# Kernel tuning notes

Hardware: AMD Instinct MI355X
Metric: run time of the kernel (lower is better)

## Reference

```python
import jax, jax.numpy as jnp
import numpy as np

N, E = 20000, 640000
D_IN, D_H, D_OUT = 128, 64, 32


def _lin_w(key, out_d, in_d):
    return jax.random.normal(key, (out_d, in_d), jnp.float32) / np.sqrt(in_d)


def setup_inputs() -> dict:
    key = jax.random.key(0)
    ks = jax.random.split(key, 16)
    x = jax.random.normal(ks[0], (N, D_IN), jnp.float32)
    edge_index = jax.random.randint(ks[1], (2, E), 0, N, jnp.int64)
    inp = {"x": x, "edge_index": edge_index}
    # SAGEConv weights: lin_l (aggregated neighbors, with bias), lin_r (root, no bias)
    inp["Wl1"] = _lin_w(ks[2], D_H, D_IN); inp["bl1"] = jnp.zeros((D_H,), jnp.float32)
    inp["Wr1"] = _lin_w(ks[3], D_H, D_IN)
    inp["Wl2"] = _lin_w(ks[4], D_H, D_H); inp["bl2"] = jnp.zeros((D_H,), jnp.float32)
    inp["Wr2"] = _lin_w(ks[5], D_H, D_H)
    inp["Wl3"] = _lin_w(ks[6], D_OUT, D_H); inp["bl3"] = jnp.zeros((D_OUT,), jnp.float32)
    inp["Wr3"] = _lin_w(ks[7], D_OUT, D_H)
    # Conv2d kernels (OIHW), all 3x3 pad 1
    inp["Wc1"] = jax.random.normal(ks[8], (D_H, 1, 3, 3), jnp.float32) / 3.0
    inp["bc1"] = jnp.zeros((D_H,), jnp.float32)
    inp["Wc2"] = jax.random.normal(ks[9], (D_H, D_H, 3, 3), jnp.float32) / np.sqrt(9 * D_H)
    inp["bc2"] = jnp.zeros((D_H,), jnp.float32)
    inp["Wc3"] = jax.random.normal(ks[10], (1, D_H, 3, 3), jnp.float32) / np.sqrt(9 * D_H)
    inp["bc3"] = jnp.zeros((1,), jnp.float32)
    # linear2 (hidden -> hidden)
    inp["W2"] = _lin_w(ks[11], D_H, D_H); inp["b2"] = jnp.zeros((D_H,), jnp.float32)
    return inp


def _sage(x, src, dst, Wl, bl, Wr):
    # PyG SAGEConv (mean aggr): lin_l(mean_{j->i} x_j) + lin_r(x_i)
    msg = x[src]  # [E, d] gather
    agg = jax.ops.segment_sum(msg, dst, num_segments=N)
    deg = jax.ops.segment_sum(jnp.ones((src.shape[0], 1), x.dtype), dst, num_segments=N)
    agg = agg / jnp.maximum(deg, 1.0)
    return agg @ Wl.T + bl + x @ Wr.T


def _conv(x, w, b):
    y = jax.lax.conv_general_dilated(x, w, (1, 1), ((1, 1), (1, 1)),
                                     dimension_numbers=("NCHW", "OIHW", "NCHW"))
    return y + b[None, :, None, None]


def reference(x, edge_index, Wl1, bl1, Wr1, Wl2, bl2, Wr2, Wl3, bl3, Wr3,
              Wc1, bc1, Wc2, bc2, Wc3, bc3, W2, b2):
    src, dst = edge_index[0], edge_index[1]
    h = _sage(x, src, dst, Wl1, bl1, Wr1)
    h = _sage(h, src, dst, Wl2, bl2, Wr2)
    h = _sage(h, src, dst, Wl2, bl2, Wr2)  # sage2 reused, as in source
    out_1 = h
    h4 = h[None, None]                     # [1,1,N,D_H]
    out = _conv(h4, Wc1, bc1)              # [1,D_H,N,D_H]
    out = _conv(out, Wc2, bc2)             # dropout is identity at inference
    out = _conv(out, Wc3, bc3)             # [1,1,N,D_H]
    out = out[0, 0] + out_1
    out = out @ W2.T + b2
    h = _sage(out, src, dst, Wl2, bl2, Wr2)
    h = _sage(h, src, dst, Wl2, bl2, Wr2)
    h = _sage(h, src, dst, Wl3, bl3, Wr3)
    return h
```

## Files before the change

### kernel.cpp

```cpp
#include <hip/hip_runtime.h>

#define NN 20000
#define NE 640000
#define NBUK 79

__device__ __forceinline__ int probe_stride(const int* __restrict__ ei32) {
  int lane = threadIdx.x & 63;
  int v = ei32[2 * lane + 1];
  unsigned long long nz = __ballot(v != 0);
  return (nz == 0ull) ? 2 : 1;
}

__device__ __forceinline__ bool maskB(int var, int o2, int o1) {
  int s = o2 + o1;
  switch (var) {
    case 0: return (o2 >= 0) && (s >= 0);
    case 1: return s >= -1;
    case 3: return s <= 1;
    case 4: return (o2 <= 0) && (s <= 0);
    default: return true;
  }
}

__global__ __launch_bounds__(256) void k_phaseA1(
    const int* __restrict__ ei, int* __restrict__ bhist,
    const float* __restrict__ Wc1, const float* __restrict__ Wc2,
    const float* __restrict__ Wc3, const float* __restrict__ bc1,
    const float* __restrict__ bc2, const float* __restrict__ bc3,
    const float* __restrict__ Wl1, const float* __restrict__ Wr1,
    const float* __restrict__ Wl2, const float* __restrict__ Wr2,
    const float* __restrict__ bl2,
    float* __restrict__ T729, float* __restrict__ beta5,
    float* __restrict__ Wt1, float* __restrict__ Wt2,
    float* __restrict__ Sbuf, float* __restrict__ c5,
    int* __restrict__ rowptr, int E, int N) {
  __shared__ float smem[6336];
  int b = blockIdx.x, tid = threadIdx.x;
  if (b >= 151) {
    int* lb = (int*)smem;
    int st = probe_stride(ei);
    for (int i = tid; i < NBUK; i += 256) lb[i] = 0;
    __syncthreads();
    int u = b - 151;
    int e0 = u * 4096;
#pragma unroll
    for (int t = 0; t < 16; ++t) {
      int e = e0 + t * 256 + tid;
      if (e < E) atomicAdd(&lb[ei[(size_t)(E + e) * st] >> 8], 1);
    }
    __syncthreads();
    for (int i = tid; i < NBUK; i += 256) bhist[u * NBUK + i] = lb[i];
    return;
  }
  int s = b;
  if (s == 0) {
    float* W3  = smem;
    float* S9s = smem + 576;
    float* W1s = smem + 5760;
    if (tid == 0) rowptr[N] = E;
    for (int e = tid; e < 576; e += 256) { W3[e] = Wc3[e]; W1s[e] = Wc1[e]; }
    __syncthreads();
    for (int bb = tid; bb < 576; bb += 256) {
      float acc[9];
#pragma unroll
      for (int a = 0; a < 9; ++a) acc[a] = 0.0f;
#pragma unroll 4
      for (int o = 0; o < 64; ++o) {
        float w2 = Wc2[o * 576 + bb];
#pragma unroll
        for (int a = 0; a < 9; ++a) acc[a] += W3[o * 9 + a] * w2;
      }
#pragma unroll
      for (int a = 0; a < 9; ++a) S9s[a * 576 + bb] = acc[a];
    }
    __syncthreads();
    for (int c = tid; c < 729; c += 256) {
      int kx0  = c % 3;
      int dl1e = (c / 3) % 3;
      int dl2e = (c / 9) % 3;
      int ky0  = (c / 27) % 3;
      int ky1  = (c / 81) % 3;
      int ky2  = c / 243;
      const float* s9 = &S9s[(ky2 * 3 + dl2e) * 576 + ky1 * 3 + dl1e];
      const float* w1 = &W1s[ky0 * 3 + kx0];
      float t = 0.0f;
#pragma unroll 8
      for (int i = 0; i < 64; ++i) t += s9[i * 9] * w1[i * 9];
      T729[c] = t;
    }
  } else if (s <= 5) {
    float* S2   = smem;
    float* W3b  = smem + 576;
    float* B2   = smem + 1152;
    float* part = smem + 1216;
    int var = s - 1;
    for (int e = tid; e < 576; e += 256) {
      int o = e / 9, r = e - o * 9;
      float t = 0.0f;
      for (int i = 0; i < 64; ++i) t += Wc2[o * 576 + i * 9 + r] * bc1[i];
      S2[e] = t;
      W3b[e] = Wc3[e];
    }
    if (tid < 64) B2[tid] = bc2[tid];
    __syncthreads();
    int u = tid & 63, oc = tid >> 6;
    float acc = 0.0f;
    for (int ky2 = 0; ky2 < 3; ++ky2) {
      int o2 = ky2 - 1;
      bool okA = (var == 0) ? (o2 >= 0) : (var == 4) ? (o2 <= 0) : true;
      if (!okA) continue;
      for (int dl2 = -1; dl2 <= 1; ++dl2) {
        int p = u + dl2; if ((unsigned)p >= 64u) continue;
        float sel[9];
#pragma unroll
        for (int ky1 = 0; ky1 < 3; ++ky1) {
          int o1 = ky1 - 1;
          bool mb = maskB(var, o2, o1);
#pragma unroll
          for (int dl1 = -1; dl1 <= 1; ++dl1) {
            int pq = p + dl1;
            sel[ky1 * 3 + dl1 + 1] = (mb && (unsigned)pq < 64u) ? 1.0f : 0.0f;
          }
        }
#pragma unroll 4
        for (int oo = 0; oo < 16; ++oo) {
          int o = oc * 16 + oo;
          float inner = B2[o];
#pragma unroll
          for (int r = 0; r < 9; ++r) inner += S2[o * 9 + r] * sel[r];
          acc += W3b[o * 9 + ky2 * 3 + (dl2 + 1)] * inner;
        }
      }
    }
    part[tid] = acc;
    __syncthreads();
    if (tid < 64) {
      beta5[var * 64 + tid] =
          bc3[0] + part[tid] + part[64 + tid] + part[128 + tid] + part[192 + tid];
    }
  } else {
    int idx = (s - 6) * 256 + tid;
    if (idx < 16384) {
      int w = idx >> 7, u = idx & 127;
      Wt1[idx] = (u < 64) ? Wl1[u * 128 + w] : Wr1[(u - 64) * 128 + w];
    } else if (idx < 24576) {
      int t = idx - 16384;
      int w = t >> 7, u = t & 127;
      Wt2[t] = (u < 64) ? Wl2[u * 64 + w] : Wr2[(u - 64) * 64 + w];
    } else if (idx < 36864) {
      int t2 = idx - 24576;
      int m = t2 >> 12, e = t2 & 4095;
      int i = e >> 6, j = e & 63;
      float acc = 0.0f;
#pragma unroll 4
      for (int k = 0; k < 64; ++k) {
        float wlj = Wl2[j * 64 + k], wrj = Wr2[j * 64 + k];
        float wli = Wl2[k * 64 + i], wri = Wr2[k * 64 + i];
        if (m == 0) acc += wli * wlj;
        else if (m == 1) acc += wri * wlj + wli * wrj;
        else acc += wri * wrj;
      }
      Sbuf[t2] = acc;
    } else if (idx < 36928) {
      int j = idx - 36864;
      float acc = bl2[j];
      for (int i = 0; i < 64; ++i)
        acc += bl2[i] * (Wl2[j * 64 + i] + Wr2[j * 64 + i]);
      c5[j] = acc;
    }
  }
}

__global__ __launch_bounds__(256) void k_phaseA2(
    const float* __restrict__ X, const float* __restrict__ Wt1,
    float* __restrict__ yzA,
    const int* __restrict__ ei, const int* __restrict__ bhist,
    unsigned long long* __restrict__ ebuf,
    const float* __restrict__ T729, float* __restrict__ M5T,
    const float* __restrict__ Sbuf, const float* __restrict__ c5,
    const float* __restrict__ Wl3, const float* __restrict__ Wr3,
    const float* __restrict__ bl3, float* __restrict__ Gbuf,
    float* __restrict__ c32, int E, int N) {
  __shared__ float smem[2048];
  int b = blockIdx.x, tid = threadIdx.x;
  if (b < 157) {
    int* lcnt  = (int*)smem;
    int* lbase = (int*)smem + 128;
    int* sscan = (int*)smem + 256;
    int st = probe_stride(ei);
    for (int i = tid; i < NBUK; i += 256) lcnt[i] = 0;
    int tot = 0, myoff = 0;
    if (tid < NBUK) {
      for (int v = 0; v < 157; ++v) {
        int h = bhist[v * NBUK + tid];
        tot += h;
        if (v < b) myoff += h;
      }
    }
    if (tid < 128) sscan[tid] = (tid < NBUK) ? tot : 0;
    __syncthreads();
    for (int off = 1; off < 128; off <<= 1) {
      int v = 0;
      if (tid < 128 && tid >= off) v = sscan[tid - off];
      __syncthreads();
      if (tid < 128) sscan[tid] += v;
      __syncthreads();
    }
    if (tid < NBUK) lbase[tid] = (sscan[tid] - tot) + myoff;
    __syncthreads();
    int e0 = b * 4096;
    int srcv[16], dstv[16], lrank[16], bk[16];
    int n = 0;
#pragma unroll
    for (int t = 0; t < 16; ++t) {
      int e = e0 + t * 256 + tid;
      if (e < E) {
        int sv = ei[(size_t)e * st];
        int d = ei[(size_t)(E + e) * st];
        int bb = d >> 8;
        srcv[n] = sv; dstv[n] = d; bk[n] = bb;
        lrank[n] = atomicAdd(&lcnt[bb], 1);
        ++n;
      }
    }
    for (int t = 0; t < n; ++t) {
      int pos = lbase[bk[t]] + lrank[t];
      ebuf[pos] = ((unsigned long long)(unsigned)dstv[t] << 32) | (unsigned)srcv[t];
    }
  } else if (b < 219) {
    float* Ts = smem;
    for (int e = tid; e < 729; e += 256) Ts[e] = T729[e];
    __syncthreads();
    int idx = (b - 157) * 256 + tid;
    if (idx >= 15680) return;
    int jw = idx % 7;
    int u  = (idx / 7) % 64;
    int d  = (idx / 448) % 7;
    int var = idx / 3136;
    int w = u + jw - 3;
    float acc = 0.0f;
    if (w >= 0 && w < 64) {
      for (int ky2 = 0; ky2 < 3; ++ky2) {
        int o2 = ky2 - 1;
        for (int ky1 = 0; ky1 < 3; ++ky1) {
          int o1 = ky1 - 1;
          if (!maskB(var, o2, o1)) continue;
          int o0 = (d - 3) - o2 - o1;
          if (o0 < -1 || o0 > 1) continue;
          int ky0 = o0 + 1;
          int cbase = ((ky2 * 3 + ky1) * 3 + ky0) * 27;
#pragma unroll
          for (int kx0 = 0; kx0 < 3; ++kx0) {
            int jq = jw - kx0;
            if ((unsigned)jq >= 5u) continue;
            int q = u + jq - 2;
            if ((unsigned)q >= 64u) continue;
#pragma unroll
            for (int dl2e = 0; dl2e < 3; ++dl2e) {
              int p = u + dl2e - 1;
              if ((unsigned)p >= 64u) continue;
              int dl1e = jq - dl2e;
              if ((unsigned)dl1e >= 3u) continue;
              acc += Ts[cbase + dl2e * 9 + dl1e * 3 + kx0];
            }
          }
        }
      }
    }
    if (d == 3 && jw == 3) acc += 1.0f;
    M5T[(var * 49 + d * 7 + jw) * 64 + u] = acc;
  } else if (b < 252) {
    int bb = b - 219;
    if (bb < 32) {
      int idx = bb * 256 + tid;
      int kblk = idx >> 11;
      int rem = idx & 2047;
      int t = rem >> 5, j = rem & 31;
      const float* S2p = Sbuf;
      const float* S1p = Sbuf + 4096;
      const float* S0p = Sbuf + 8192;
      const float* pa = (kblk == 0) ? S2p : (kblk == 1) ? S1p : (kblk == 2) ? S0p : nullptr;
      const float* pb = (kblk == 1) ? S2p : (kblk == 2) ? S1p : (kblk == 3) ? S0p : nullptr;
      float acc = 0.0f;
#pragma unroll 4
      for (int k = 0; k < 64; ++k) {
        if (pa) acc += pa[t * 64 + k] * Wl3[j * 64 + k];
        if (pb) acc += pb[t * 64 + k] * Wr3[j * 64 + k];
      }
      Gbuf[idx] = acc;
    } else if (tid < 32) {
      float acc = bl3[tid];
      for (int k = 0; k < 64; ++k)
        acc += c5[k] * (Wl3[tid * 64 + k] + Wr3[tid * 64 + k]);
      c32[tid] = acc;
    }
  } else {
    constexpr int C = 128, K = 128, ROWS = 16, RPT = ROWS * C / 256;
    float* Xs = smem;
    int y0 = (b - 252) * ROWS;
    {
      const float4* src = (const float4*)(X + (size_t)y0 * K);
      float4* dst = (float4*)Xs;
#pragma unroll
      for (int v = 0; v < ROWS * K / 4 / 256; ++v)
        dst[v * 256 + tid] = src[v * 256 + tid];
    }
    __syncthreads();
    int u = tid % C;
    int rg = tid / C;
    float acc[RPT];
#pragma unroll
    for (int k = 0; k < RPT; ++k) acc[k] = 0.0f;
#pragma unroll 2
    for (int w0 = 0; w0 < K; w0 += 4) {
      float m0 = Wt1[(w0 + 0) * C + u];
      float m1 = Wt1[(w0 + 1) * C + u];
      float m2 = Wt1[(w0 + 2) * C + u];
      float m3 = Wt1[(w0 + 3) * C + u];
      const float* xs = &Xs[(rg * RPT) * K + w0];
#pragma unroll
      for (int k = 0; k < RPT; ++k) {
        float4 h = *(const float4*)(xs + k * K);
        acc[k] += m0 * h.x + m1 * h.y + m2 * h.z + m3 * h.w;
      }
    }
#pragma unroll
    for (int k = 0; k < RPT; ++k)
      yzA[(size_t)(y0 + rg * RPT + k) * C + u] = acc[k];
  }
}

__global__ __launch_bounds__(256) void k_phaseA3(
    const unsigned long long* __restrict__ ebuf, const int* __restrict__ bhist,
    int* __restrict__ rowptr, float* __restrict__ invdeg,
    int* __restrict__ csr,
    const float* __restrict__ Gbuf, const float* __restrict__ W2,
    const float* __restrict__ b2, float* __restrict__ Wg,
    float* __restrict__ bg, int N) {
  __shared__ int smem[772];
  int b = blockIdx.x, tid = threadIdx.x;
  if (b < NBUK) {
    int* lcnt  = smem;
    int* lcur  = smem + 256;
    int* wsum  = smem + 512;
    int* sscan = smem + 516;
    int* tots  = smem + 644;
    int tot = 0;
    if (tid < NBUK)
      for (int v = 0; v < 157; ++v) tot += bhist[v * NBUK + tid];
    if (tid < 128) { tots[tid] = (tid < NBUK) ? tot : 0; sscan[tid] = tots ? ((tid < NBUK) ? tot : 0) : 0; }
    __syncthreads();
    for (int off = 1; off < 128; off <<= 1) {
      int v = 0;
      if (tid < 128 && tid >= off) v = sscan[tid - off];
      __syncthreads();
      if (tid < 128) sscan[tid] += v;
      __syncthreads();
    }
    if (tid < 128) sscan[tid] -= tots[tid];
    __syncthreads();
    int base = sscan[b];
    int n = tots[b];
    lcnt[tid] = 0;
    __syncthreads();
    for (int e = tid; e < n; e += 256) {
      int d = (int)(ebuf[base + e] >> 32);
      atomicAdd(&lcnt[d - (b << 8)], 1);
    }
    __syncthreads();
    int c = lcnt[tid];
    int lane = tid & 63, wid = tid >> 6;
    int s = c;
#pragma unroll
    for (int off = 1; off < 64; off <<= 1) {
      int v = __shfl_up(s, off, 64);
      if (lane >= off) s += v;
    }
    if (lane == 63) wsum[wid] = s;
    __syncthreads();
    int woff = 0;
    for (int w = 0; w < wid; ++w) woff += wsum[w];
    int pref = woff + s - c;
    int gnode = (b << 8) + tid;
    if (gnode < N) {
      rowptr[gnode] = base + pref;
      invdeg[gnode] = 1.0f / (float)(c < 1 ? 1 : c);
    }
    lcur[tid] = pref;
    __syncthreads();
    for (int e = tid; e < n; e += 256) {
      unsigned long long pk = ebuf[base + e];
      int d = (int)(pk >> 32);
      int pos = atomicAdd(&lcur[d - (b << 8)], 1);
      csr[base + pos] = (int)(unsigned)pk;
    }
  } else {
    int bb = b - NBUK;
    if (bb < 32) {
      int idx = bb * 256 + tid;
      int w = idx >> 7, u = idx & 127;
      int kblk = u >> 5, j = u & 31;
      const float* gp = Gbuf + kblk * 2048 + j;
      float acc = 0.0f;
#pragma unroll 4
      for (int t = 0; t < 64; ++t) acc += W2[t * 64 + w] * gp[t * 32];
      Wg[idx] = acc;
    } else if (tid < 128) {
      int kblk = tid >> 5, j = tid & 31;
      const float* gp = Gbuf + kblk * 2048 + j;
      float acc = 0.0f;
      for (int t = 0; t < 64; ++t) acc += b2[t] * gp[t * 32];
      bg[tid] = acc;
    }
  }
}

template <int C>
__global__ __launch_bounds__(256) void k_fused(const float* __restrict__ yzin,
                                               const int* __restrict__ csr,
                                               const int* __restrict__ rowptr,
                                               const float* __restrict__ invdeg,
                                               const float* __restrict__ bl,
                                               const float* __restrict__ Wt,
                                               float* __restrict__ out, int N) {
  constexpr int FV = 16;
  constexpr int G  = 4;
  constexpr int S4 = 32;
  constexpr int CAP = 64;
  __shared__ int idxs[16 * CAP];
  __shared__ float htile[16 * 64];
  int tid = threadIdx.x;
  int w = tid >> 6, lane = tid & 63;
  int base = blockIdx.x * 16;
  int beg_r[4], m_r[4], end_r[4];
#pragma unroll
  for (int rr = 0; rr < 4; ++rr) {
    int node = base + w * 4 + rr;
    int beg = rowptr[node], end = rowptr[node + 1];
    beg_r[rr] = beg; end_r[rr] = end;
    int cnt = end - beg;
    int m = cnt < CAP ? cnt : CAP;
    m_r[rr] = m;
    int* my = &idxs[(w * 4 + rr) * CAP];
    for (int k = lane; k < m; k += 64) my[k] = csr[beg + k];
  }
  __syncthreads();
  int g = lane / FV, f = lane % FV;
  const float4* yz4 = (const float4*)yzin;
#pragma unroll
  for (int rr = 0; rr < 4; ++rr) {
    int node = base + w * 4 + rr;
    const int* my = &idxs[(w * 4 + rr) * CAP];
    int m = m_r[rr];
    float a0x=0,a0y=0,a0z=0,a0w=0, a1x=0,a1y=0,a1z=0,a1w=0;
    float a2x=0,a2y=0,a2z=0,a2w=0, a3x=0,a3y=0,a3z=0,a3w=0;
    int j = g;
    for (; j + 3 * G < m; j += 4 * G) {
      int s0 = my[j], s1 = my[j + G], s2 = my[j + 2 * G], s3 = my[j + 3 * G];
      float4 v0 = yz4[(size_t)s0 * S4 + f];
      float4 v1 = yz4[(size_t)s1 * S4 + f];
      float4 v2 = yz4[(size_t)s2 * S4 + f];
      float4 v3 = yz4[(size_t)s3 * S4 + f];
      a0x += v0.x; a0y += v0.y; a0z += v0.z; a0w += v0.w;
      a1x += v1.x; a1y += v1.y; a1z += v1.z; a1w += v1.w;
      a2x += v2.x; a2y += v2.y; a2z += v2.z; a2w += v2.w;
      a3x += v3.x; a3y += v3.y; a3z += v3.z; a3w += v3.w;
    }
    for (; j < m; j += G) {
      int s0 = my[j];
      float4 v0 = yz4[(size_t)s0 * S4 + f];
      a0x += v0.x; a0y += v0.y; a0z += v0.z; a0w += v0.w;
    }
    for (int jj = beg_r[rr] + CAP + g; jj < end_r[rr]; jj += G) {
      int s0 = csr[jj];
      float4 v0 = yz4[(size_t)s0 * S4 + f];
      a0x += v0.x; a0y += v0.y; a0z += v0.z; a0w += v0.w;
    }
    float ax = (a0x + a1x) + (a2x + a3x);
    float ay = (a0y + a1y) + (a2y + a3y);
    float az = (a0z + a1z) + (a2z + a3z);
    float aw = (a0w + a1w) + (a2w + a3w);
#pragma unroll
    for (int mm = FV; mm < 64; mm <<= 1) {
      ax += __shfl_xor(ax, mm, 64);
      ay += __shfl_xor(ay, mm, 64);
      az += __shfl_xor(az, mm, 64);
      aw += __shfl_xor(aw, mm, 64);
    }
    if (g == 0) {
      float4 root = yz4[(size_t)node * S4 + FV + f];
      float4 bv = ((const float4*)bl)[f];
      float id = invdeg[node];
      float4 o;
      o.x = ax * id + bv.x + root.x;
      o.y = ay * id + bv.y + root.y;
      o.z = az * id + bv.z + root.z;
      o.w = aw * id + bv.w + root.w;
      ((float4*)htile)[(w * 4 + rr) * 16 + f] = o;
    }
  }
  __syncthreads();
  constexpr int RPT = 16 * C / 256;
  int u = tid % C, rg = tid / C;
  float acc[RPT];
#pragma unroll
  for (int k = 0; k < RPT; ++k) acc[k] = 0.0f;
#pragma unroll 2
  for (int w0 = 0; w0 < 64; w0 += 4) {
    float m0 = Wt[(w0 + 0) * C + u];
    float m1 = Wt[(w0 + 1) * C + u];
    float m2 = Wt[(w0 + 2) * C + u];
    float m3 = Wt[(w0 + 3) * C + u];
    const float* xs = &htile[(rg * RPT) * 64 + w0];
#pragma unroll
    for (int k = 0; k < RPT; ++k) {
      float4 h4 = *(const float4*)(xs + k * 64);
      acc[k] += m0 * h4.x + m1 * h4.y + m2 * h4.z + m3 * h4.w;
    }
  }
#pragma unroll
  for (int k = 0; k < RPT; ++k)
    out[(size_t)(base + rg * RPT + k) * C + u] = acc[k];
}

__global__ __launch_bounds__(256) void k_applyfused(
    const float* __restrict__ h, const float* __restrict__ M5T,
    const float* __restrict__ beta5, const float* __restrict__ Wg,
    const float* __restrict__ bg, float* __restrict__ wout, int N) {
  __shared__ float hs[22 * 70];
  __shared__ float htile[16 * 64];
  int tid = threadIdx.x;
  int bstart = blockIdx.x * 16;
  for (int idx = tid; idx < 22 * 70; idx += 256) {
    int row = idx / 70, col = idx - row * 70;
    int y = bstart - 3 + row;
    int ww = col - 3;
    float v = 0.0f;
    if ((unsigned)y < (unsigned)N && (unsigned)ww < 64u)
      v = h[(size_t)y * 64 + ww];
    hs[idx] = v;
  }
  __syncthreads();
  int u = tid & 63, g = tid >> 6;
  int lr0 = g * 4;
  int gstart = bstart + lr0;
  const float* basep = &hs[lr0 * 70 + u];
  bool interior = (gstart >= 2) && (gstart + 3 <= N - 3);
  if (interior) {
    float c[49];
#pragma unroll
    for (int t = 0; t < 49; ++t) c[t] = M5T[(2 * 49 + t) * 64 + u];
    float bet = beta5[2 * 64 + u];
    float acc[4];
#pragma unroll
    for (int k = 0; k < 4; ++k) acc[k] = bet;
#pragma unroll
    for (int rr = 0; rr < 10; ++rr) {
      float t7[7];
#pragma unroll
      for (int jw = 0; jw < 7; ++jw) t7[jw] = basep[rr * 70 + jw];
#pragma unroll
      for (int d = 0; d < 7; ++d) {
        int k = rr - d;
        if (k >= 0 && k < 4) {
#pragma unroll
          for (int jw = 0; jw < 7; ++jw) acc[k] += c[d * 7 + jw] * t7[jw];
        }
      }
    }
#pragma unroll
    for (int k = 0; k < 4; ++k) htile[(lr0 + k) * 64 + u] = acc[k];
  } else {
    for (int k = 0; k < 4; ++k) {
      int y = gstart + k;
      int var = (y == 0) ? 0 : (y == 1) ? 1 : (y == N - 2) ? 3 : (y == N - 1) ? 4 : 2;
      float acc = beta5[var * 64 + u];
      for (int d = 0; d < 7; ++d)
        for (int jw = 0; jw < 7; ++jw)
          acc += M5T[(var * 49 + d * 7 + jw) * 64 + u] * basep[(k + d) * 70 + jw];
      htile[(lr0 + k) * 64 + u] = acc;
    }
  }
  __syncthreads();
  int u2 = tid % 128, rg = tid / 128;
  float acc2[8];
  float bv = bg[u2];
#pragma unroll
  for (int k = 0; k < 8; ++k) acc2[k] = bv;
#pragma unroll 2
  for (int w0 = 0; w0 < 64; w0 += 4) {
    float m0 = Wg[(w0 + 0) * 128 + u2];
    float m1 = Wg[(w0 + 1) * 128 + u2];
    float m2 = Wg[(w0 + 2) * 128 + u2];
    float m3 = Wg[(w0 + 3) * 128 + u2];
    const float* xs = &htile[(rg * 8) * 64 + w0];
#pragma unroll
    for (int k = 0; k < 8; ++k) {
      float4 h4 = *(const float4*)(xs + k * 64);
      acc2[k] += m0 * h4.x + m1 * h4.y + m2 * h4.z + m3 * h4.w;
    }
  }
  int kb = u2 >> 5, jj = u2 & 31;
#pragma unroll
  for (int k = 0; k < 8; ++k) {
    int node = bstart + rg * 8 + k;
    wout[((size_t)kb * N + node) * 32 + jj] = acc2[k];
  }
}

template <int DH>
__global__ __launch_bounds__(256) void k_agg(const float* __restrict__ yz,
                                             const int* __restrict__ csr,
                                             const int* __restrict__ rowptr,
                                             const float* __restrict__ invdeg,
                                             const float* __restrict__ bl,
                                             float* __restrict__ out, int N) {
  constexpr int FV = DH / 4;
  constexpr int G  = 64 / FV;
  constexpr int S4 = DH / 2;
  constexpr int CAP = 256;
  __shared__ int idxs[4 * CAP];
  int wid = threadIdx.x >> 6, lane = threadIdx.x & 63;
  int node = blockIdx.x * 4 + wid;
  int beg = rowptr[node], end = rowptr[node + 1];
  int cnt = end - beg;
  int m = cnt < CAP ? cnt : CAP;
  int* my = &idxs[wid * CAP];
  for (int k = lane; k < m; k += 64) my[k] = csr[beg + k];
  __syncthreads();
  int g = lane / FV, f = lane % FV;
  const float4* yz4 = (const float4*)yz;
  float a0x=0,a0y=0,a0z=0,a0w=0, a1x=0,a1y=0,a1z=0,a1w=0;
  float a2x=0,a2y=0,a2z=0,a2w=0, a3x=0,a3y=0,a3z=0,a3w=0;
  int j = g;
  for (; j + 3 * G < m; j += 4 * G) {
    int s0 = my[j], s1 = my[j + G], s2 = my[j + 2 * G], s3 = my[j + 3 * G];
    float4 v0 = yz4[(size_t)s0 * S4 + f];
    float4 v1 = yz4[(size_t)s1 * S4 + f];
    float4 v2 = yz4[(size_t)s2 * S4 + f];
    float4 v3 = yz4[(size_t)s3 * S4 + f];
    a0x += v0.x; a0y += v0.y; a0z += v0.z; a0w += v0.w;
    a1x += v1.x; a1y += v1.y; a1z += v1.z; a1w += v1.w;
    a2x += v2.x; a2y += v2.y; a2z += v2.z; a2w += v2.w;
    a3x += v3.x; a3y += v3.y; a3z += v3.z; a3w += v3.w;
  }
  for (; j < m; j += G) {
    int s0 = my[j];
    float4 v0 = yz4[(size_t)s0 * S4 + f];
    a0x += v0.x; a0y += v0.y; a0z += v0.z; a0w += v0.w;
  }
  for (int jj = beg + CAP + g; jj < end; jj += G) {
    int s0 = csr[jj];
    float4 v0 = yz4[(size_t)s0 * S4 + f];
    a0x += v0.x; a0y += v0.y; a0z += v0.z; a0w += v0.w;
  }
  float ax = (a0x + a1x) + (a2x + a3x);
  float ay = (a0y + a1y) + (a2y + a3y);
  float az = (a0z + a1z) + (a2z + a3z);
  float aw = (a0w + a1w) + (a2w + a3w);
#pragma unroll
  for (int mm = FV; mm < 64; mm <<= 1) {
    ax += __shfl_xor(ax, mm, 64);
    ay += __shfl_xor(ay, mm, 64);
    az += __shfl_xor(az, mm, 64);
    aw += __shfl_xor(aw, mm, 64);
  }
  if (g == 0) {
    float4 root = yz4[(size_t)node * S4 + FV + f];
    float4 bv = ((const float4*)bl)[f];
    float id = invdeg[node];
    float4 o;
    o.x = ax * id + bv.x + root.x;
    o.y = ay * id + bv.y + root.y;
    o.z = az * id + bv.z + root.z;
    o.w = aw * id + bv.w + root.w;
    ((float4*)out)[(size_t)node * FV + f] = o;
  }
}

__global__ __launch_bounds__(256) void k_agg32(
    const float* __restrict__ src, const int* __restrict__ csr,
    const int* __restrict__ rowptr, const float* __restrict__ invdeg,
    const float* __restrict__ add, const float* __restrict__ cvec,
    float* __restrict__ out, int N) {
  constexpr int FV = 8;
  constexpr int G  = 8;
  constexpr int CAP = 256;
  __shared__ int idxs[4 * CAP];
  int wid = threadIdx.x >> 6, lane = threadIdx.x & 63;
  int node = blockIdx.x * 4 + wid;
  int beg = rowptr[node], end = rowptr[node + 1];
  int cnt = end - beg;
  int m = cnt < CAP ? cnt : CAP;
  int* my = &idxs[wid * CAP];
  for (int k = lane; k < m; k += 64) my[k] = csr[beg + k];
  __syncthreads();
  int g = lane / FV, f = lane % FV;
  const float4* sr4 = (const float4*)src;
  float a0x=0,a0y=0,a0z=0,a0w=0, a1x=0,a1y=0,a1z=0,a1w=0;
  float a2x=0,a2y=0,a2z=0,a2w=0, a3x=0,a3y=0,a3z=0,a3w=0;
  int j = g;
  for (; j + 3 * G < m; j += 4 * G) {
    int s0 = my[j], s1 = my[j + G], s2 = my[j + 2 * G], s3 = my[j + 3 * G];
    float4 v0 = sr4[(size_t)s0 * FV + f];
    float4 v1 = sr4[(size_t)s1 * FV + f];
    float4 v2 = sr4[(size_t)s2 * FV + f];
    float4 v3 = sr4[(size_t)s3 * FV + f];
    a0x += v0.x; a0y += v0.y; a0z += v0.z; a0w += v0.w;
    a1x += v1.x; a1y += v1.y; a1z += v1.z; a1w += v1.w;
    a2x += v2.x; a2y += v2.y; a2z += v2.z; a2w += v2.w;
    a3x += v3.x; a3y += v3.y; a3z += v3.z; a3w += v3.w;
  }
  for (; j < m; j += G) {
    int s0 = my[j];
    float4 v0 = sr4[(size_t)s0 * FV + f];
    a0x += v0.x; a0y += v0.y; a0z += v0.z; a0w += v0.w;
  }
  for (int jj = beg + CAP + g; jj < end; jj += G) {
    int s0 = csr[jj];
    float4 v0 = sr4[(size_t)s0 * FV + f];
    a0x += v0.x; a0y += v0.y; a0z += v0.z; a0w += v0.w;
  }
  float ax = (a0x + a1x) + (a2x + a3x);
  float ay = (a0y + a1y) + (a2y + a3y);
  float az = (a0z + a1z) + (a2z + a3z);
  float aw = (a0w + a1w) + (a2w + a3w);
#pragma unroll
  for (int mm = FV; mm < 64; mm <<= 1) {
    ax += __shfl_xor(ax, mm, 64);
    ay += __shfl_xor(ay, mm, 64);
    az += __shfl_xor(az, mm, 64);
    aw += __shfl_xor(aw, mm, 64);
  }
  if (g == 0) {
    float4 av = ((const float4*)add)[(size_t)node * FV + f];
    float id = invdeg[node];
    float4 o;
    o.x = ax * id + av.x;
    o.y = ay * id + av.y;
    o.z = az * id + av.z;
    o.w = aw * id + av.w;
    if (cvec != nullptr) {
      float4 cv = ((const float4*)cvec)[f];
      o.x += cv.x; o.y += cv.y; o.z += cv.z; o.w += cv.w;
    }
    ((float4*)out)[(size_t)node * FV + f] = o;
  }
}

extern "C" void kernel_launch(void* const* d_in, const int* in_sizes, int n_in,
                              void* d_out, int out_size, void* d_ws, size_t ws_size,
                              hipStream_t stream) {
  const int N = NN, E = NE;
  const float* x   = (const float*)d_in[0];
  const int*   ei  = (const int*)d_in[1];
  const float* Wl1 = (const float*)d_in[2];
  const float* bl1 = (const float*)d_in[3];
  const float* Wr1 = (const float*)d_in[4];
  const float* Wl2 = (const float*)d_in[5];
  const float* bl2 = (const float*)d_in[6];
  const float* Wr2 = (const float*)d_in[7];
  const float* Wl3 = (const float*)d_in[8];
  const float* bl3 = (const float*)d_in[9];
  const float* Wr3 = (const float*)d_in[10];
  const float* Wc1 = (const float*)d_in[11];
  const float* bc1 = (const float*)d_in[12];
  const float* Wc2 = (const float*)d_in[13];
  const float* bc2 = (const float*)d_in[14];
  const float* Wc3 = (const float*)d_in[15];
  const float* bc3 = (const float*)d_in[16];
  const float* W2  = (const float*)d_in[17];
  const float* b2  = (const float*)d_in[18];

  char* ws = (char*)d_ws;
  size_t off = 0;
  auto alloc = [&](size_t bytes) -> void* {
    off = (off + 255) & ~(size_t)255;
    void* p = ws + off;
    off += bytes;
    return p;
  };
  int*   rowptr  = (int*)alloc((size_t)(N + 1) * 4);
  float* invdeg  = (float*)alloc((size_t)N * 4);
  int*   csr     = (int*)alloc((size_t)E * 4);
  unsigned long long* ebuf = (unsigned long long*)alloc((size_t)E * 8);
  int*   bhist   = (int*)alloc(157 * NBUK * 4);
  float* Wt1     = (float*)alloc(128 * 128 * 4);
  float* Wt2     = (float*)alloc(64 * 128 * 4);
  float* T729    = (float*)alloc(729 * 4);
  float* M5T     = (float*)alloc(15680 * 4);
  float* beta5   = (float*)alloc(320 * 4);
  float* Sbuf    = (float*)alloc(12288 * 4);
  float* c5      = (float*)alloc(64 * 4);
  float* Gbuf    = (float*)alloc(8192 * 4);
  float* Wg      = (float*)alloc(8192 * 4);
  float* bg      = (float*)alloc(128 * 4);
  float* c32     = (float*)alloc(32 * 4);
  float* yzA     = (float*)alloc((size_t)N * 128 * 4);
  float* yzB     = (float*)alloc((size_t)N * 128 * 4);
  float* hA      = (float*)alloc((size_t)N * 64 * 4);
  float* wbuf    = (float*)alloc((size_t)4 * N * 32 * 4);
  float* s1buf   = (float*)alloc((size_t)N * 32 * 4);
  float* s2buf   = (float*)alloc((size_t)N * 32 * 4);
  (void)ws_size; (void)in_sizes; (void)n_in; (void)out_size;

  const int gG = N / 16;
  const int gA = N / 4;

  k_phaseA1<<<308, 256, 0, stream>>>(ei, bhist, Wc1, Wc2, Wc3, bc1, bc2, bc3,
                                     Wl1, Wr1, Wl2, Wr2, bl2,
                                     T729, beta5, Wt1, Wt2, Sbuf, c5,
                                     rowptr, E, N);
  k_phaseA2<<<1502, 256, 0, stream>>>(x, Wt1, yzA, ei, bhist, ebuf,
                                      T729, M5T, Sbuf, c5, Wl3, Wr3, bl3,
                                      Gbuf, c32, E, N);
  k_phaseA3<<<112, 256, 0, stream>>>(ebuf, bhist, rowptr, invdeg, csr,
                                     Gbuf, W2, b2, Wg, bg, N);

  k_fused<128><<<gG, 256, 0, stream>>>(yzA, csr, rowptr, invdeg, bl1, Wt2, yzB, N);
  k_fused<128><<<gG, 256, 0, stream>>>(yzB, csr, rowptr, invdeg, bl2, Wt2, yzA, N);
  k_agg<64><<<gA, 256, 0, stream>>>(yzA, csr, rowptr, invdeg, bl2, hA, N);
  k_applyfused<<<gG, 256, 0, stream>>>(hA, M5T, beta5, Wg, bg, wbuf, N);
  const float* w3  = wbuf;
  const float* w2p = wbuf + (size_t)N * 32;
  const float* w1p = wbuf + (size_t)2 * N * 32;
  const float* w0p = wbuf + (size_t)3 * N * 32;
  k_agg32<<<gA, 256, 0, stream>>>(w3, csr, rowptr, invdeg, w2p, nullptr, s1buf, N);
  k_agg32<<<gA, 256, 0, stream>>>(s1buf, csr, rowptr, invdeg, w1p, nullptr, s2buf, N);
  k_agg32<<<gA, 256, 0, stream>>>(s2buf, csr, rowptr, invdeg, w0p, c32, (float*)d_out, N);
}
```

Baseline: 278.6 us.

## Bin edges into fixed-capacity per-block cells and merge CSR build into phaseA2

The histogram blocks in phaseA1 now also write each packed (dst,src) edge into a fixed-size cell indexed by (edge block, destination bucket). That removes the separate global scatter pass that used to read edge_index a second time. phaseA2's first 79 blocks then assemble each bucket directly from these cells, using a prefix scan and binary search, to produce rowptr, invdeg and csr. The Gbuf, Wg and bg weight folding is done by a single block, so the third setup kernel launch is gone. The trade-off is that the code assumes no (block, bucket) cell exceeds 128 edges, which holds only for roughly uniform destinations, and it adds serial work in one block.

Result: slower. 676.3 us (+142.7%).

```diff
diff --git a/kernel.cpp b/kernel.cpp
--- a/kernel.cpp
+++ b/kernel.cpp
@@ -3,6 +3,8 @@
 #define NN 20000
 #define NE 640000
 #define NBUK 79
+#define NPB 157
+#define CELL 128
 
 __device__ __forceinline__ int probe_stride(const int* __restrict__ ei32) {
   int lane = threadIdx.x & 63;
@@ -24,6 +26,7 @@
 
 __global__ __launch_bounds__(256) void k_phaseA1(
     const int* __restrict__ ei, int* __restrict__ bhist,
+    unsigned long long* __restrict__ ebuf2,
     const float* __restrict__ Wc1, const float* __restrict__ Wc2,
     const float* __restrict__ Wc3, const float* __restrict__ bc1,
     const float* __restrict__ bc2, const float* __restrict__ bc3,
@@ -37,19 +40,25 @@
   __shared__ float smem[6336];
   int b = blockIdx.x, tid = threadIdx.x;
   if (b >= 151) {
-    int* lb = (int*)smem;
+    int* lcnt = (int*)smem;
     int st = probe_stride(ei);
-    for (int i = tid; i < NBUK; i += 256) lb[i] = 0;
+    for (int i = tid; i < NBUK; i += 256) lcnt[i] = 0;
     __syncthreads();
     int u = b - 151;
     int e0 = u * 4096;
-#pragma unroll
     for (int t = 0; t < 16; ++t) {
       int e = e0 + t * 256 + tid;
-      if (e < E) atomicAdd(&lb[ei[(size_t)(E + e) * st] >> 8], 1);
-    }
-    __syncthreads();
-    for (int i = tid; i < NBUK; i += 256) bhist[u * NBUK + i] = lb[i];
+      if (e < E) {
+        int sv = ei[(size_t)e * st];
+        int d  = ei[(size_t)(E + e) * st];
+        int bb = d >> 8;
+        int r = atomicAdd(&lcnt[bb], 1);
+        ebuf2[((size_t)u * NBUK + bb) * CELL + r] =
+            ((unsigned long long)(unsigned)d << 32) | (unsigned)sv;
+      }
+    }
+    __syncthreads();
+    for (int i = tid; i < NBUK; i += 256) bhist[u * NBUK + i] = lcnt[i];
     return;
   }
   int s = b;
@@ -174,31 +183,48 @@
 __global__ __launch_bounds__(256) void k_phaseA2(
     const float* __restrict__ X, const float* __restrict__ Wt1,
     float* __restrict__ yzA,
-    const int* __restrict__ ei, const int* __restrict__ bhist,
-    unsigned long long* __restrict__ ebuf,
+    const unsigned long long* __restrict__ ebuf2,
+    const int* __restrict__ bhist,
+    int* __restrict__ rowptr, float* __restrict__ invdeg,
+    int* __restrict__ csr,
     const float* __restrict__ T729, float* __restrict__ M5T,
     const float* __restrict__ Sbuf, const float* __restrict__ c5,
     const float* __restrict__ Wl3, const float* __restrict__ Wr3,
     const float* __restrict__ bl3, float* __restrict__ Gbuf,
+    float* __restrict__ Wg, float* __restrict__ bg,
+    const float* __restrict__ W2, const float* __restrict__ b2,
     float* __restrict__ c32, int E, int N) {
   __shared__ float smem[2048];
   int b = blockIdx.x, tid = threadIdx.x;
-  if (b < 157) {
-    int* lcnt  = (int*)smem;
-    int* lbase = (int*)smem + 128;
-    int* sscan = (int*)smem + 256;
-    int st = probe_stride(ei);
-    for (int i = tid; i < NBUK; i += 256) lcnt[i] = 0;
-    int tot = 0, myoff = 0;
-    if (tid < NBUK) {
-      for (int v = 0; v < 157; ++v) {
-        int h = bhist[v * NBUK + tid];
-        tot += h;
-        if (v < b) myoff += h;
+  if (b < NBUK) {
+    int* lens  = (int*)smem;
+    int* cs    = (int*)smem + 160;
+    int* lcnt  = (int*)smem + 416;
+    int* lcur  = (int*)smem + 672;
+    int* wsum  = (int*)smem + 928;
+    int* sscan = (int*)smem + 932;
+    int* tots  = (int*)smem + 1060;
+    if (tid < 160) lens[tid] = (tid < NPB) ? bhist[tid * NBUK + b] : 0;
+    int tot = 0;
+    if (tid < NBUK)
+      for (int v = 0; v < NPB; ++v) tot += bhist[v * NBUK + tid];
+    if (tid < 128) {
+      int tv = (tid < NBUK) ? tot : 0;
+      tots[tid] = tv;
+      sscan[tid] = tv;
+    }
+    __syncthreads();
+    {
+      int mine = (tid < NPB) ? lens[tid] : 0;
+      cs[tid] = mine;
+      __syncthreads();
+      for (int off = 1; off < 256; off <<= 1) {
+        int v = (tid >= off) ? cs[tid - off] : 0;
+        __syncthreads();
+        cs[tid] += v;
+        __syncthreads();
       }
     }
-    if (tid < 128) sscan[tid] = (tid < NBUK) ? tot : 0;
-    __syncthreads();
     for (int off = 1; off < 128; off <<= 1) {
       int v = 0;
       if (tid < 128 && tid >= off) v = sscan[tid - off];
@@ -206,32 +232,53 @@
       if (tid < 128) sscan[tid] += v;
       __syncthreads();
     }
-    if (tid < NBUK) lbase[tid] = (sscan[tid] - tot) + myoff;
-    __syncthreads();
-    int e0 = b * 4096;
-    int srcv[16], dstv[16], lrank[16], bk[16];
-    int n = 0;
-#pragma unroll
-    for (int t = 0; t < 16; ++t) {
-      int e = e0 + t * 256 + tid;
-      if (e < E) {
-        int sv = ei[(size_t)e * st];
-        int d = ei[(size_t)(E + e) * st];
-        int bb = d >> 8;
-        srcv[n] = sv; dstv[n] = d; bk[n] = bb;
-        lrank[n] = atomicAdd(&lcnt[bb], 1);
-        ++n;
-      }
-    }
-    for (int t = 0; t < n; ++t) {
-      int pos = lbase[bk[t]] + lrank[t];
-      ebuf[pos] = ((unsigned long long)(unsigned)dstv[t] << 32) | (unsigned)srcv[t];
-    }
-  } else if (b < 219) {
+    if (tid < 128) sscan[tid] -= tots[tid];
+    lcnt[tid] = 0;
+    __syncthreads();
+    int base = sscan[b];
+    int n = cs[NPB - 1];
+    for (int i = tid; i < n; i += 256) {
+      int lo = 0, hi = NPB - 1;
+      while (lo < hi) { int mid = (lo + hi) >> 1; if (cs[mid] > i) hi = mid; else lo = mid + 1; }
+      int pos = i - (cs[lo] - lens[lo]);
+      unsigned long long pk = ebuf2[((size_t)lo * NBUK + b) * CELL + pos];
+      atomicAdd(&lcnt[(int)(pk >> 32) & 255], 1);
+    }
+    __syncthreads();
+    int c = lcnt[tid];
+    int lane = tid & 63, wid = tid >> 6;
+    int sacc = c;
+#pragma unroll
+    for (int off = 1; off < 64; off <<= 1) {
+      int v = __shfl_up(sacc, off, 64);
+      if (lane >= off) sacc += v;
+    }
+    if (lane == 63) wsum[wid] = sacc;
+    __syncthreads();
+    int woff = 0;
+    for (int w = 0; w < wid; ++w) woff += wsum[w];
+    int pref = woff + sacc - c;
+    int gnode = (b << 8) + tid;
+    if (gnode < N) {
+      rowptr[gnode] = base + pref;
+      invdeg[gnode] = 1.0f / (float)(c < 1 ? 1 : c);
+    }
+    lcur[tid] = pref;
+    __syncthreads();
+    for (int i = tid; i < n; i += 256) {
+      int lo = 0, hi = NPB - 1;
+      while (lo < hi) { int mid = (lo + hi) >> 1; if (cs[mid] > i) hi = mid; else lo = mid + 1; }
+      int pos = i - (cs[lo] - lens[lo]);
+      unsigned long long pk = ebuf2[((size_t)lo * NBUK + b) * CELL + pos];
+      int d = (int)(pk >> 32);
+      int p2 = atomicAdd(&lcur[d & 255], 1);
+      csr[base + p2] = (int)(unsigned)pk;
+    }
+  } else if (b < 141) {
     float* Ts = smem;
     for (int e = tid; e < 729; e += 256) Ts[e] = T729[e];
     __syncthreads();
-    int idx = (b - 157) * 256 + tid;
+    int idx = (b - NBUK) * 256 + tid;
     if (idx >= 15680) return;
     int jw = idx % 7;
     int u  = (idx / 7) % 64;
@@ -269,10 +316,8 @@
     }
     if (d == 3 && jw == 3) acc += 1.0f;
     M5T[(var * 49 + d * 7 + jw) * 64 + u] = acc;
-  } else if (b < 252) {
-    int bb = b - 219;
-    if (bb < 32) {
-      int idx = bb * 256 + tid;
+  } else if (b == 141) {
+    for (int idx = tid; idx < 8192; idx += 256) {
       int kblk = idx >> 11;
       int rem = idx & 2047;
       int t = rem >> 5, j = rem & 31;
@@ -288,7 +333,25 @@
         if (pb) acc += pb[t * 64 + k] * Wr3[j * 64 + k];
       }
       Gbuf[idx] = acc;
-    } else if (tid < 32) {
+    }
+    __syncthreads();
+    for (int idx = tid; idx < 8192; idx += 256) {
+      int w = idx >> 7, u = idx & 127;
+      int kblk = u >> 5, j = u & 31;
+      const float* gp = Gbuf + kblk * 2048 + j;
+      float acc = 0.0f;
+#pragma unroll 4
+      for (int t = 0; t < 64; ++t) acc += W2[t * 64 + w] * gp[t * 32];
+      Wg[idx] = acc;
+    }
+    if (tid < 128) {
+      int kblk = tid >> 5, j = tid & 31;
+      const float* gp = Gbuf + kblk * 2048 + j;
+      float acc = 0.0f;
+      for (int t = 0; t < 64; ++t) acc += b2[t] * gp[t * 32];
+      bg[tid] = acc;
+    }
+    if (tid < 32) {
       float acc = bl3[tid];
       for (int k = 0; k < 64; ++k)
         acc += c5[k] * (Wl3[tid * 64 + k] + Wr3[tid * 64 + k]);
@@ -297,7 +360,7 @@
   } else {
     constexpr int C = 128, K = 128, ROWS = 16, RPT = ROWS * C / 256;
     float* Xs = smem;
-    int y0 = (b - 252) * ROWS;
+    int y0 = (b - 142) * ROWS;
     {
       const float4* src = (const float4*)(X + (size_t)y0 * K);
       float4* dst = (float4*)Xs;
@@ -327,91 +390,6 @@
 #pragma unroll
     for (int k = 0; k < RPT; ++k)
       yzA[(size_t)(y0 + rg * RPT + k) * C + u] = acc[k];
-  }
-}
-
-__global__ __launch_bounds__(256) void k_phaseA3(
-    const unsigned long long* __restrict__ ebuf, const int* __restrict__ bhist,
-    int* __restrict__ rowptr, float* __restrict__ invdeg,
-    int* __restrict__ csr,
-    const float* __restrict__ Gbuf, const float* __restrict__ W2,
-    const float* __restrict__ b2, float* __restrict__ Wg,
-    float* __restrict__ bg, int N) {
-  __shared__ int smem[772];
-  int b = blockIdx.x, tid = threadIdx.x;
-  if (b < NBUK) {
-    int* lcnt  = smem;
-    int* lcur  = smem + 256;
-    int* wsum  = smem + 512;
-    int* sscan = smem + 516;
-    int* tots  = smem + 644;
-    int tot = 0;
-    if (tid < NBUK)
-      for (int v = 0; v < 157; ++v) tot += bhist[v * NBUK + tid];
-    if (tid < 128) { tots[tid] = (tid < NBUK) ? tot : 0; sscan[tid] = tots ? ((tid < NBUK) ? tot : 0) : 0; }
-    __syncthreads();
-    for (int off = 1; off < 128; off <<= 1) {
-      int v = 0;
-      if (tid < 128 && tid >= off) v = sscan[tid - off];
-      __syncthreads();
-      if (tid < 128) sscan[tid] += v;
-      __syncthreads();
-    }
-    if (tid < 128) sscan[tid] -= tots[tid];
-    __syncthreads();
-    int base = sscan[b];
-    int n = tots[b];
-    lcnt[tid] = 0;
-    __syncthreads();
-    for (int e = tid; e < n; e += 256) {
-      int d = (int)(ebuf[base + e] >> 32);
-      atomicAdd(&lcnt[d - (b << 8)], 1);
-    }
-    __syncthreads();
-    int c = lcnt[tid];
-    int lane = tid & 63, wid = tid >> 6;
-    int s = c;
-#pragma unroll
-    for (int off = 1; off < 64; off <<= 1) {
-      int v = __shfl_up(s, off, 64);
-      if (lane >= off) s += v;
-    }
-    if (lane == 63) wsum[wid] = s;
-    __syncthreads();
-    int woff = 0;
-    for (int w = 0; w < wid; ++w) woff += wsum[w];
-    int pref = woff + s - c;
-    int gnode = (b << 8) + tid;
-    if (gnode < N) {
-      rowptr[gnode] = base + pref;
-      invdeg[gnode] = 1.0f / (float)(c < 1 ? 1 : c);
-    }
-    lcur[tid] = pref;
-    __syncthreads();
-    for (int e = tid; e < n; e += 256) {
-      unsigned long long pk = ebuf[base + e];
-      int d = (int)(pk >> 32);
-      int pos = atomicAdd(&lcur[d - (b << 8)], 1);
-      csr[base + pos] = (int)(unsigned)pk;
-    }
-  } else {
-    int bb = b - NBUK;
-    if (bb < 32) {
-      int idx = bb * 256 + tid;
-      int w = idx >> 7, u = idx & 127;
-      int kblk = u >> 5, j = u & 31;
-      const float* gp = Gbuf + kblk * 2048 + j;
-      float acc = 0.0f;
-#pragma unroll 4
-      for (int t = 0; t < 64; ++t) acc += W2[t * 64 + w] * gp[t * 32];
-      Wg[idx] = acc;
-    } else if (tid < 128) {
-      int kblk = tid >> 5, j = tid & 31;
-      const float* gp = Gbuf + kblk * 2048 + j;
-      float acc = 0.0f;
-      for (int t = 0; t < 64; ++t) acc += b2[t] * gp[t * 32];
-      bg[tid] = acc;
-    }
   }
 }
 
@@ -783,8 +761,9 @@
   int*   rowptr  = (int*)alloc((size_t)(N + 1) * 4);
   float* invdeg  = (float*)alloc((size_t)N * 4);
   int*   csr     = (int*)alloc((size_t)E * 4);
-  unsigned long long* ebuf = (unsigned long long*)alloc((size_t)E * 8);
-  int*   bhist   = (int*)alloc(157 * NBUK * 4);
+  unsigned long long* ebuf2 =
+      (unsigned long long*)alloc((size_t)NPB * NBUK * CELL * 8);
+  int*   bhist   = (int*)alloc(NPB * NBUK * 4);
   float* Wt1     = (float*)alloc(128 * 128 * 4);
   float* Wt2     = (float*)alloc(64 * 128 * 4);
   float* T729    = (float*)alloc(729 * 4);
@@ -807,15 +786,15 @@
   const int gG = N / 16;
   const int gA = N / 4;
 
-  k_phaseA1<<<308, 256, 0, stream>>>(ei, bhist, Wc1, Wc2, Wc3, bc1, bc2, bc3,
+  k_phaseA1<<<308, 256, 0, stream>>>(ei, bhist, ebuf2,
+                                     Wc1, Wc2, Wc3, bc1, bc2, bc3,
                                      Wl1, Wr1, Wl2, Wr2, bl2,
                                      T729, beta5, Wt1, Wt2, Sbuf, c5,
                                      rowptr, E, N);
-  k_phaseA2<<<1502, 256, 0, stream>>>(x, Wt1, yzA, ei, bhist, ebuf,
+  k_phaseA2<<<1392, 256, 0, stream>>>(x, Wt1, yzA, ebuf2, bhist,
+                                      rowptr, invdeg, csr,
                                       T729, M5T, Sbuf, c5, Wl3, Wr3, bl3,
-                                      Gbuf, c32, E, N);
-  k_phaseA3<<<112, 256, 0, stream>>>(ebuf, bhist, rowptr, invdeg, csr,
-                                     Gbuf, W2, b2, Wg, bg, N);
+                                      Gbuf, Wg, bg, W2, b2, c32, E, N);
 
   k_fused<128><<<gG, 256, 0, stream>>>(yzA, csr, rowptr, invdeg, bl1, Wt2, yzB, N);
   k_fused<128><<<gG, 256, 0, stream>>>(yzB, csr, rowptr, invdeg, bl2, Wt2, yzA, N);
```
